# Performance work log

Measured on AMD Instinct MI355X. Metric: run time of the kernel, lower is better.

## Reference

```python
import jax, jax.numpy as jnp
import numpy as np

DEPTH = 2
DIM = 256
MLP = 1024
B = 2
N = 2048


def setup_inputs() -> dict:
    key = jax.random.key(0)
    ks = jax.random.split(key, 6)
    s = 0.02
    d = DIM
    f32 = jnp.float32
    return {
        "x": jax.random.normal(ks[0], (B, N, d), f32),
        "ln1_g": jnp.ones((DEPTH, d), f32),
        "ln1_b": jnp.zeros((DEPTH, d), f32),
        "Wqkv": (jax.random.normal(ks[1], (DEPTH, d, 3 * d), f32) * s),
        "bqkv": jnp.zeros((DEPTH, 3 * d), f32),
        "Wo": (jax.random.normal(ks[2], (DEPTH, d, d), f32) * s),
        "bo": jnp.zeros((DEPTH, d), f32),
        "ln2_g": jnp.ones((DEPTH, d), f32),
        "ln2_b": jnp.zeros((DEPTH, d), f32),
        "W1": (jax.random.normal(ks[3], (DEPTH, d, MLP), f32) * s),
        "b1": jnp.zeros((DEPTH, MLP), f32),
        "W2": (jax.random.normal(ks[4], (DEPTH, MLP, d), f32) * s),
        "b2": jnp.zeros((DEPTH, d), f32),
        "heads": 8,
    }


def _ln(x, g, b, eps=1e-5):
    m = x.mean(-1, keepdims=True)
    v = ((x - m) ** 2).mean(-1, keepdims=True)
    return (x - m) * jax.lax.rsqrt(v + eps) * g + b


def reference(x, ln1_g, ln1_b, Wqkv, bqkv, Wo, bo, ln2_g, ln2_b, W1, b1, W2, b2, heads):
    b, n, dim = x.shape
    hd = dim // heads
    scale = hd ** -0.5
    depth = Wqkv.shape[0]
    out = x
    # NOTE: faithful to original: `x` is never updated inside the loop,
    # so only the last layer's output is returned.
    for i in range(depth):
        y = _ln(x, ln1_g[i], ln1_b[i])
        qkv = y @ Wqkv[i] + bqkv[i]                      # [b,n,3*dim]
        qkv = qkv.reshape(b, n, 3, heads, hd)
        q, k, v = jnp.moveaxis(qkv, 2, 0)                # each [b,n,h,hd]
        q = q.transpose(0, 2, 1, 3)                      # [b,h,n,hd]
        k = k.transpose(0, 2, 1, 3)
        v = v.transpose(0, 2, 1, 3)
        dots = jnp.einsum('bhid,bhjd->bhij', q, k) * scale
        attn = jax.nn.softmax(dots, axis=-1)
        o = jnp.einsum('bhij,bhjd->bhid', attn, v)       # [b,h,n,hd]
        o = o.transpose(0, 2, 1, 3).reshape(b, n, dim)
        o = o @ Wo[i] + bo[i]
        a = o + x                                        # attn residual
        z = _ln(a, ln2_g[i], ln2_b[i])
        m = jax.nn.gelu(z @ W1[i] + b1[i], approximate=False) @ W2[i] + b2[i]
        out = m + a                                      # mlp residual
    return out
```

## Files before the change

### kernel.cpp

```cpp
#include <hip/hip_runtime.h>
#include <hip/hip_bf16.h>
#include <math.h>

#define DEPTHC 2
#define DIMD   256
#define MLPD   1024
#define BB     2
#define NN     2048
#define HH     8
#define HD     32
#define ROWS   (BB * NN)
#define KSPLIT 4

typedef __attribute__((ext_vector_type(8))) short bf16x8;
typedef __attribute__((ext_vector_type(4))) float f32x4;

__device__ __forceinline__ short f2bf(float x) {
    union { float f; unsigned u; } c; c.f = x;
    unsigned u = c.u + (0x7fffu + ((c.u >> 16) & 1u));
    return (short)(u >> 16);
}
__device__ __forceinline__ float bf2f(short s) {
    union { unsigned u; float f; } c; c.u = ((unsigned)(unsigned short)s) << 16;
    return c.f;
}

__global__ __launch_bounds__(256) void prep(
    const float* __restrict__ Wqkv, const float* __restrict__ Wo,
    const float* __restrict__ W1,   const float* __restrict__ W2,
    short* __restrict__ WqkvF, short* __restrict__ WoF,
    short* __restrict__ W1F,   short* __restrict__ W2F,
    const float* __restrict__ x, const float* __restrict__ g,
    const float* __restrict__ be, short* __restrict__ y)
{
    __shared__ short Ts[128][72];

    if (blockIdx.x >= 96) {
        const int wave = threadIdx.x >> 6;
        const int lane = threadIdx.x & 63;
        const int row  = (blockIdx.x - 96) * 4 + wave;
        const int c    = lane * 4;

        const float4 v = *(const float4*)&x[(size_t)row * DIMD + c];
        float s  = v.x + v.y + v.z + v.w;
        float sq = v.x * v.x + v.y * v.y + v.z * v.z + v.w * v.w;
#pragma unroll
        for (int off = 32; off > 0; off >>= 1) {
            s  += __shfl_down(s,  off, 64);
            sq += __shfl_down(sq, off, 64);
        }
        s  = __shfl(s,  0, 64);
        sq = __shfl(sq, 0, 64);

        const float mean = s * (1.f / DIMD);
        const float var  = sq * (1.f / DIMD) - mean * mean;
        const float rstd = rsqrtf(var + 1e-5f);

        const float4 gg = *(const float4*)&g[c];
        const float4 bb = *(const float4*)&be[c];
        short4 ov;
        ov.x = f2bf((v.x - mean) * rstd * gg.x + bb.x);
        ov.y = f2bf((v.y - mean) * rstd * gg.y + bb.y);
        ov.z = f2bf((v.z - mean) * rstd * gg.z + bb.z);
        ov.w = f2bf((v.w - mean) * rstd * gg.w + bb.w);
        *(short4*)&y[(size_t)row * DIMD + c] = ov;
        return;
    }

    int blk = blockIdx.x;
    const float* W; short* WF; int K, N;
    if (blk < 24)      {           W = Wqkv; WF = WqkvF; K = 256;  N = 768;  }
    else if (blk < 32) { blk -= 24; W = Wo;   WF = WoF;   K = 256;  N = 256;  }
    else if (blk < 64) { blk -= 32; W = W1;   WF = W1F;   K = 256;  N = 1024; }
    else               { blk -= 64; W = W2;   WF = W2F;   K = 1024; N = 256;  }
    const int nkc = K >> 7;
    const int bx  = blk / nkc;
    const int kc  = blk % nkc;
    const int n0  = bx * 64;
    const int k0  = kc * 128;

    const int nc  = threadIdx.x & 63;
    const int kr0 = threadIdx.x >> 6;
#pragma unroll
    for (int i = 0; i < 32; ++i) {
        const int kr = kr0 + i * 4;
        Ts[kr][nc] = f2bf(W[(size_t)(k0 + kr) * N + n0 + nc]);
    }
    __syncthreads();

    short* out = WF + ((size_t)bx * nkc + kc) * 8192;
#pragma unroll
    for (int i = 0; i < 4; ++i) {
        const int u    = threadIdx.x + i * 256;
        const int l16  = u & 15;
        const int quad = (u >> 4) & 3;
        const int nt   = (u >> 6) & 3;
        const int ks   = (u >> 8) & 3;
        const int n    = nt * 16 + l16;
        const int kk   = (ks * 4 + quad) * 8;
        bf16x8 v;
#pragma unroll
        for (int j = 0; j < 8; ++j) v[j] = Ts[kk + j][n];
        *(bf16x8*)&out[(size_t)u * 8] = v;
    }
}

template <int K, bool GELU, bool RES, bool OBF, bool VTG, bool MERGE>
__global__ __launch_bounds__(256) void gemm_ks(
    const short* __restrict__ A, const short* __restrict__ WF,
    const float* __restrict__ bias, const float* __restrict__ R,
    void* __restrict__ Cv, int N, short* __restrict__ vtg,
    const short* __restrict__ pO, const float* __restrict__ pl)
{
    __shared__ short smem[4][4096];

    const int tid  = threadIdx.x;
    const int w    = tid >> 6;
    const int lane = tid & 63;
    const int quad = lane >> 4;
    const int l16  = lane & 15;
    const int n0   = blockIdx.x * 64;
    const int m0   = blockIdx.y * 64;
    constexpr int NKC   = K / 128;
    constexpr int SLICE = K / 4;
    constexpr int NHC   = SLICE / 64;

    const short* wfb  = WF + (size_t)blockIdx.x * NKC * 8192;
    const short* arow = (MERGE ? pO : A) ? ((MERGE ? pO : A) + (size_t)(m0 + l16) * K + quad * 8)
                                         : nullptr;
    short* reg = smem[w];

    f32x4 acc[4][4] = {};

#pragma unroll
    for (int hc = 0; hc < NHC; ++hc) {
        const int kbase = w * SLICE + hc * 64;
        const short* src = wfb +
            ((size_t)(kbase >> 7) * 1024 + (size_t)((kbase >> 6) & 1) * 512) * 8;
#pragma unroll
        for (int i = 0; i < 8; ++i)
            *(bf16x8*)&reg[(i * 64 + lane) * 8] =
                *(const bf16x8*)&src[(size_t)(i * 64 + lane) * 8];

#pragma unroll
        for (int ksl = 0; ksl < 2; ++ksl) {
            const int kk = kbase + ksl * 32;
            bf16x8 af[4];
#pragma unroll
            for (int mt = 0; mt < 4; ++mt) {
                if (!MERGE) {
                    af[mt] = *(const bf16x8*)(arow + (size_t)mt * 16 * K + kk);
                } else {
                    const int row = m0 + l16 + mt * 16;
                    const int c   = kk + quad * 8;
                    const int h   = c >> 5;
                    const int d0  = c & 31;
                    const int b   = row >> 11;
                    const int q   = row & (NN - 1);
                    const size_t rg = ((size_t)(b * HH + h) * NN + q) * KSPLIT;
                    const float L = pl[rg] + pl[rg + 1] + pl[rg + 2] + pl[rg + 3];
                    float o[8] = {};
#pragma unroll
                    for (int s = 0; s < KSPLIT; ++s) {
                        const bf16x8 t = *(const bf16x8*)&pO[(rg + s) * HD + d0];
#pragma unroll
                        for (int j = 0; j < 8; ++j) o[j] += bf2f(t[j]);
                    }
                    const float inv = 1.f / L;
#pragma unroll
                    for (int j = 0; j < 8; ++j) af[mt][j] = f2bf(o[j] * inv);
                }
            }
#pragma unroll
            for (int nt = 0; nt < 4; ++nt) {
                const bf16x8 bf = *(const bf16x8*)
                    &reg[(((ksl * 4 + nt) * 4 + quad) * 16 + l16) * 8];
#pragma unroll
                for (int mt = 0; mt < 4; ++mt)
                    acc[mt][nt] = __builtin_amdgcn_mfma_f32_16x16x32_bf16(
                        af[mt], bf, acc[mt][nt], 0, 0, 0);
            }
        }
    }

#pragma unroll
    for (int p = 0; p < 2; ++p) {
        __syncthreads();
#pragma unroll
        for (int mtl = 0; mtl < 2; ++mtl)
#pragma unroll
            for (int nt = 0; nt < 4; ++nt)
                *(f32x4*)&smem[w][((mtl * 4 + nt) * 64 + lane) * 8] = acc[2 * p + mtl][nt];
        __syncthreads();
        if ((w >> 1) == p) {
            const int mtl = w & 1;
            const int mt  = 2 * p + mtl;
#pragma unroll
            for (int nt = 0; nt < 4; ++nt) {
                const int idx = ((mtl * 4 + nt) * 64 + lane) * 8;
                const f32x4 s0 = *(const f32x4*)&smem[0][idx];
                const f32x4 s1 = *(const f32x4*)&smem[1][idx];
                const f32x4 s2 = *(const f32x4*)&smem[2][idx];
                const f32x4 s3 = *(const f32x4*)&smem[3][idx];
                const f32x4 s  = (s0 + s1) + (s2 + s3);
                const int col  = n0 + nt * 16 + l16;
                const float bb = bias[col];
#pragma unroll
                for (int r = 0; r < 4; ++r) {
                    const int row = m0 + mt * 16 + quad * 4 + r;
                    float v = s[r] + bb;
                    if (RES)  v += R[(size_t)row * N + col];
                    if (GELU) v = 0.5f * v * (1.f + erff(v * 0.70710678118f));
                    const short bv = f2bf(v);
                    if (OBF) ((short*)Cv)[(size_t)row * N + col] = bv;
                    else     ((float*)Cv)[(size_t)row * N + col] = v;
                    if (VTG && n0 >= 2 * DIMD) {
                        const int vc = col - 2 * DIMD;
                        const int b  = row >> 11;
                        const int q  = row & (NN - 1);
                        const int h  = vc >> 5;
                        const int d  = vc & 31;
                        vtg[((size_t)(b * HH + h) * HD + d) * NN + q] = bv;
                    }
                }
            }
        }
    }
}

__global__ __launch_bounds__(256) void ln_kernel(
    const float* __restrict__ x, const float* __restrict__ g,
    const float* __restrict__ bta, short* __restrict__ y)
{
    const int wave = threadIdx.x >> 6;
    const int lane = threadIdx.x & 63;
    const int row  = blockIdx.x * 4 + wave;
    const int c    = lane * 4;

    const float4 v = *(const float4*)&x[(size_t)row * DIMD + c];
    float s  = v.x + v.y + v.z + v.w;
    float sq = v.x * v.x + v.y * v.y + v.z * v.z + v.w * v.w;
#pragma unroll
    for (int off = 32; off > 0; off >>= 1) {
        s  += __shfl_down(s,  off, 64);
        sq += __shfl_down(sq, off, 64);
    }
    s  = __shfl(s,  0, 64);
    sq = __shfl(sq, 0, 64);

    const float mean = s * (1.f / DIMD);
    const float var  = sq * (1.f / DIMD) - mean * mean;
    const float rstd = rsqrtf(var + 1e-5f);

    const float4 gg = *(const float4*)&g[c];
    const float4 bb = *(const float4*)&bta[c];
    short4 ov;
    ov.x = f2bf((v.x - mean) * rstd * gg.x + bb.x);
    ov.y = f2bf((v.y - mean) * rstd * gg.y + bb.y);
    ov.z = f2bf((v.z - mean) * rstd * gg.z + bb.z);
    ov.w = f2bf((v.w - mean) * rstd * gg.w + bb.w);
    *(short4*)&y[(size_t)row * DIMD + c] = ov;
}

__global__ __launch_bounds__(256) void attn_mfma(
    const short* __restrict__ qkv, const short* __restrict__ vtg,
    short* __restrict__ pO, float* __restrict__ pl)
{
    __shared__ short Ks[64][40];
    __shared__ short Vs[32][72];
    __shared__ short Ps[4][16][72];

    const int tid  = threadIdx.x;
    const int w    = tid >> 6;
    const int lane = tid & 63;
    const int quad = lane >> 4;
    const int l16  = lane & 15;
    const int bh   = blockIdx.y;
    const int b    = bh >> 3;
    const int h    = bh & 7;
    const int ks   = blockIdx.z;
    const int q0   = blockIdx.x * 64 + w * 16;

    const float scale2 = 0.25504606868000365f;
    const short* base = qkv + (size_t)b * NN * (3 * DIMD);

    const bf16x8 qfrag =
        *(const bf16x8*)(base + (size_t)(q0 + l16) * (3 * DIMD) + h * HD + quad * 8);

    const int skey = tid >> 2;
    const int sd   = (tid & 3) * 8;
    const int vd   = tid >> 3;
    const int vk   = (tid & 7) * 8;

    const short* kgp = base + (size_t)(ks * (NN / KSPLIT) + skey) * (3 * DIMD)
                       + DIMD + h * HD + sd;
    const short* vgp = vtg + ((size_t)bh * HD + vd) * NN
                       + ks * (NN / KSPLIT) + vk;

    f32x4 oacc0 = {0.f, 0.f, 0.f, 0.f};
    f32x4 oacc1 = {0.f, 0.f, 0.f, 0.f};
    float rowsum[4] = {0.f, 0.f, 0.f, 0.f};

    bf16x8 kreg = *(const bf16x8*)kgp;
    bf16x8 vreg = *(const bf16x8*)vgp;

#pragma unroll 1
    for (int t = 0; t < NN / KSPLIT / 64; ++t) {
        __syncthreads();
        *(bf16x8*)&Ks[skey][sd] = kreg;
        *(bf16x8*)&Vs[vd][vk]   = vreg;
        __syncthreads();

        if (t + 1 < NN / KSPLIT / 64) {
            kreg = *(const bf16x8*)(kgp + (size_t)(t + 1) * 64 * (3 * DIMD));
            vreg = *(const bf16x8*)(vgp + (t + 1) * 64);
        }

        f32x4 s[4];
#pragma unroll
        for (int kt = 0; kt < 4; ++kt) {
            const bf16x8 kf = *(const bf16x8*)&Ks[kt * 16 + l16][quad * 8];
            f32x4 z = {0.f, 0.f, 0.f, 0.f};
            s[kt] = __builtin_amdgcn_mfma_f32_16x16x32_bf16(qfrag, kf, z, 0, 0, 0);
        }

#pragma unroll
        for (int kt = 0; kt < 4; ++kt)
#pragma unroll
            for (int r = 0; r < 4; ++r) {
                const float p = exp2f(fmaf(s[kt][r], scale2, -16.f));
                rowsum[r] += p;
                union { float f; unsigned u; } cv; cv.f = p;
                Ps[w][quad * 4 + r][kt * 16 + l16] = (short)(cv.u >> 16);
            }

#pragma unroll
        for (int c = 0; c < 2; ++c) {
            const bf16x8 pf = *(const bf16x8*)&Ps[w][l16][c * 32 + quad * 8];
            const bf16x8 v0 = *(const bf16x8*)&Vs[l16][c * 32 + quad * 8];
            const bf16x8 v1 = *(const bf16x8*)&Vs[16 + l16][c * 32 + quad * 8];
            oacc0 = __builtin_amdgcn_mfma_f32_16x16x32_bf16(pf, v0, oacc0, 0, 0, 0);
            oacc1 = __builtin_amdgcn_mfma_f32_16x16x32_bf16(pf, v1, oacc1, 0, 0, 0);
        }
    }

#pragma unroll
    for (int off = 1; off <= 8; off <<= 1)
#pragma unroll
        for (int r = 0; r < 4; ++r)
            rowsum[r] += __shfl_xor(rowsum[r], off, 64);

#pragma unroll
    for (int r = 0; r < 4; ++r) {
        const size_t rg = (size_t)bh * NN + q0 + quad * 4 + r;
        pO[(rg * KSPLIT + ks) * HD + l16]      = f2bf(oacc0[r]);
        pO[(rg * KSPLIT + ks) * HD + 16 + l16] = f2bf(oacc1[r]);
        if (l16 == 0) pl[rg * KSPLIT + ks] = rowsum[r];
    }
}

extern "C" void kernel_launch(void* const* d_in, const int* in_sizes, int n_in,
                              void* d_out, int out_size, void* d_ws, size_t ws_size,
                              hipStream_t stream)
{
    const int L = DEPTHC - 1;
    const float* x     = (const float*)d_in[0];
    const float* ln1_g = (const float*)d_in[1]  + L * DIMD;
    const float* ln1_b = (const float*)d_in[2]  + L * DIMD;
    const float* Wqkv  = (const float*)d_in[3]  + (size_t)L * DIMD * 3 * DIMD;
    const float* bqkv  = (const float*)d_in[4]  + L * 3 * DIMD;
    const float* Wo    = (const float*)d_in[5]  + (size_t)L * DIMD * DIMD;
    const float* bo    = (const float*)d_in[6]  + L * DIMD;
    const float* ln2_g = (const float*)d_in[7]  + L * DIMD;
    const float* ln2_b = (const float*)d_in[8]  + L * DIMD;
    const float* W1    = (const float*)d_in[9]  + (size_t)L * DIMD * MLPD;
    const float* b1    = (const float*)d_in[10] + L * MLPD;
    const float* W2    = (const float*)d_in[11] + (size_t)L * MLPD * DIMD;
    const float* b2    = (const float*)d_in[12] + L * DIMD;
    float* out = (float*)d_out;

    short* WqkvF = (short*)d_ws;
    short* WoF   = WqkvF + 12 * 2 * 8192;
    short* W1F   = WoF   + 4 * 2 * 8192;
    short* W2F   = W1F   + 16 * 2 * 8192;
    short* ybf   = W2F   + 4 * 8 * 8192;
    short* zbf   = ybf   + (size_t)ROWS * DIMD;
    short* qkvbf = zbf   + (size_t)ROWS * DIMD;
    short* vtg   = qkvbf + (size_t)ROWS * 3 * DIMD;
    short* pO    = vtg   + (size_t)16 * HD * NN;
    short* m1bf  = pO    + (size_t)16 * NN * KSPLIT * HD;
    float* pl    = (float*)(m1bf + (size_t)ROWS * MLPD);
    float* a     = pl + (size_t)16 * NN * KSPLIT;

    prep<<<96 + ROWS / 4, 256, 0, stream>>>(
        Wqkv, Wo, W1, W2, WqkvF, WoF, W1F, W2F, x, ln1_g, ln1_b, ybf);

    gemm_ks<256, false, false, true, true, false><<<dim3(12, 64), 256, 0, stream>>>(
        ybf, WqkvF, bqkv, nullptr, qkvbf, 3 * DIMD, vtg, nullptr, nullptr);

    attn_mfma<<<dim3(NN / 64, BB * HH, KSPLIT), 256, 0, stream>>>(qkvbf, vtg, pO, pl);

    gemm_ks<256, false, true, false, false, true><<<dim3(4, 64), 256, 0, stream>>>(
        nullptr, WoF, bo, x, a, DIMD, nullptr, pO, pl);

    ln_kernel<<<ROWS / 4, 256, 0, stream>>>(a, ln2_g, ln2_b, zbf);

    gemm_ks<256, true, false, true, false, false><<<dim3(16, 64), 256, 0, stream>>>(
        zbf, W1F, b1, nullptr, m1bf, MLPD, nullptr, nullptr, nullptr);

    gemm_ks<1024, false, true, false, false, false><<<dim3(4, 64), 256, 0, stream>>>(
        m1bf, W2F, b2, a, out, DIMD, nullptr, nullptr, nullptr);
}
```

Before: 169.1 us.

## Fuse attention merge, out-proj, LN2 and MLP into one tail kernel

Replaces the four post-attention launches (Wo GEMM with split-K merge, LN2, W1 GEMM with GELU, W2 GEMM) with a single kernel that handles 32 rows per block. The residual, the LN2 output and the GELU activations stay in registers and LDS. This removes the global round trips for a, zbf and the 4096x1024 m1 intermediate, along with three launches. In exchange there are only 128 blocks, so per-CU parallelism is lower, and every block re-streams all of Wo, W1 and W2 from global memory.

```diff
diff --git a/kernel.cpp b/kernel.cpp
--- a/kernel.cpp
+++ b/kernel.cpp
@@ -11,6 +11,7 @@
 #define HD     32
 #define ROWS   (BB * NN)
 #define KSPLIT 4
+#define TM     32
 
 typedef __attribute__((ext_vector_type(8))) short bf16x8;
 typedef __attribute__((ext_vector_type(4))) float f32x4;
@@ -105,14 +106,13 @@
     }
 }
 
-template <int K, bool GELU, bool RES, bool OBF, bool VTG, bool MERGE>
-__global__ __launch_bounds__(256) void gemm_ks(
+__global__ __launch_bounds__(256) void gemm_qkv(
     const short* __restrict__ A, const short* __restrict__ WF,
-    const float* __restrict__ bias, const float* __restrict__ R,
-    void* __restrict__ Cv, int N, short* __restrict__ vtg,
-    const short* __restrict__ pO, const float* __restrict__ pl)
+    const float* __restrict__ bias, short* __restrict__ Cv,
+    short* __restrict__ vtg)
 {
     __shared__ short smem[4][4096];
+    constexpr int K = 256, N = 3 * DIMD;
 
     const int tid  = threadIdx.x;
     const int w    = tid >> 6;
@@ -121,56 +121,28 @@
     const int l16  = lane & 15;
     const int n0   = blockIdx.x * 64;
     const int m0   = blockIdx.y * 64;
-    constexpr int NKC   = K / 128;
-    constexpr int SLICE = K / 4;
-    constexpr int NHC   = SLICE / 64;
-
-    const short* wfb  = WF + (size_t)blockIdx.x * NKC * 8192;
-    const short* arow = (MERGE ? pO : A) ? ((MERGE ? pO : A) + (size_t)(m0 + l16) * K + quad * 8)
-                                         : nullptr;
+
+    const short* wfb  = WF + (size_t)blockIdx.x * 2 * 8192;
+    const short* arow = A + (size_t)(m0 + l16) * K + quad * 8;
     short* reg = smem[w];
 
     f32x4 acc[4][4] = {};
 
-#pragma unroll
-    for (int hc = 0; hc < NHC; ++hc) {
-        const int kbase = w * SLICE + hc * 64;
-        const short* src = wfb +
-            ((size_t)(kbase >> 7) * 1024 + (size_t)((kbase >> 6) & 1) * 512) * 8;
+    {
+        const int kbase = w * 64;
+        const short* src = wfb + ((size_t)(kbase >> 7) * 1024
+                                  + (size_t)((kbase >> 6) & 1) * 512) * 8;
 #pragma unroll
         for (int i = 0; i < 8; ++i)
             *(bf16x8*)&reg[(i * 64 + lane) * 8] =
                 *(const bf16x8*)&src[(size_t)(i * 64 + lane) * 8];
-
 #pragma unroll
         for (int ksl = 0; ksl < 2; ++ksl) {
             const int kk = kbase + ksl * 32;
             bf16x8 af[4];
 #pragma unroll
-            for (int mt = 0; mt < 4; ++mt) {
-                if (!MERGE) {
-                    af[mt] = *(const bf16x8*)(arow + (size_t)mt * 16 * K + kk);
-                } else {
-                    const int row = m0 + l16 + mt * 16;
-                    const int c   = kk + quad * 8;
-                    const int h   = c >> 5;
-                    const int d0  = c & 31;
-                    const int b   = row >> 11;
-                    const int q   = row & (NN - 1);
-                    const size_t rg = ((size_t)(b * HH + h) * NN + q) * KSPLIT;
-                    const float L = pl[rg] + pl[rg + 1] + pl[rg + 2] + pl[rg + 3];
-                    float o[8] = {};
-#pragma unroll
-                    for (int s = 0; s < KSPLIT; ++s) {
-                        const bf16x8 t = *(const bf16x8*)&pO[(rg + s) * HD + d0];
-#pragma unroll
-                        for (int j = 0; j < 8; ++j) o[j] += bf2f(t[j]);
-                    }
-                    const float inv = 1.f / L;
-#pragma unroll
-                    for (int j = 0; j < 8; ++j) af[mt][j] = f2bf(o[j] * inv);
-                }
-            }
+            for (int mt = 0; mt < 4; ++mt)
+                af[mt] = *(const bf16x8*)(arow + (size_t)mt * 16 * K + kk);
 #pragma unroll
             for (int nt = 0; nt < 4; ++nt) {
                 const bf16x8 bf = *(const bf16x8*)
@@ -208,58 +180,18 @@
 #pragma unroll
                 for (int r = 0; r < 4; ++r) {
                     const int row = m0 + mt * 16 + quad * 4 + r;
-                    float v = s[r] + bb;
-                    if (RES)  v += R[(size_t)row * N + col];
-                    if (GELU) v = 0.5f * v * (1.f + erff(v * 0.70710678118f));
-                    const short bv = f2bf(v);
-                    if (OBF) ((short*)Cv)[(size_t)row * N + col] = bv;
-                    else     ((float*)Cv)[(size_t)row * N + col] = v;
-                    if (VTG && n0 >= 2 * DIMD) {
+                    const short bv = f2bf(s[r] + bb);
+                    Cv[(size_t)row * N + col] = bv;
+                    if (n0 >= 2 * DIMD) {
                         const int vc = col - 2 * DIMD;
                         const int b  = row >> 11;
                         const int q  = row & (NN - 1);
-                        const int h  = vc >> 5;
-                        const int d  = vc & 31;
-                        vtg[((size_t)(b * HH + h) * HD + d) * NN + q] = bv;
+                        vtg[((size_t)(b * HH + (vc >> 5)) * HD + (vc & 31)) * NN + q] = bv;
                     }
                 }
             }
         }
     }
-}
-
-__global__ __launch_bounds__(256) void ln_kernel(
-    const float* __restrict__ x, const float* __restrict__ g,
-    const float* __restrict__ bta, short* __restrict__ y)
-{
-    const int wave = threadIdx.x >> 6;
-    const int lane = threadIdx.x & 63;
-    const int row  = blockIdx.x * 4 + wave;
-    const int c    = lane * 4;
-
-    const float4 v = *(const float4*)&x[(size_t)row * DIMD + c];
-    float s  = v.x + v.y + v.z + v.w;
-    float sq = v.x * v.x + v.y * v.y + v.z * v.z + v.w * v.w;
-#pragma unroll
-    for (int off = 32; off > 0; off >>= 1) {
-        s  += __shfl_down(s,  off, 64);
-        sq += __shfl_down(sq, off, 64);
-    }
-    s  = __shfl(s,  0, 64);
-    sq = __shfl(sq, 0, 64);
-
-    const float mean = s * (1.f / DIMD);
-    const float var  = sq * (1.f / DIMD) - mean * mean;
-    const float rstd = rsqrtf(var + 1e-5f);
-
-    const float4 gg = *(const float4*)&g[c];
-    const float4 bb = *(const float4*)&bta[c];
-    short4 ov;
-    ov.x = f2bf((v.x - mean) * rstd * gg.x + bb.x);
-    ov.y = f2bf((v.y - mean) * rstd * gg.y + bb.y);
-    ov.z = f2bf((v.z - mean) * rstd * gg.z + bb.z);
-    ov.w = f2bf((v.w - mean) * rstd * gg.w + bb.w);
-    *(short4*)&y[(size_t)row * DIMD + c] = ov;
 }
 
 __global__ __launch_bounds__(256) void attn_mfma(
@@ -356,6 +288,208 @@
         pO[(rg * KSPLIT + ks) * HD + l16]      = f2bf(oacc0[r]);
         pO[(rg * KSPLIT + ks) * HD + 16 + l16] = f2bf(oacc1[r]);
         if (l16 == 0) pl[rg * KSPLIT + ks] = rowsum[r];
+    }
+}
+
+__global__ __launch_bounds__(256) void tail(
+    const short* __restrict__ pO, const float* __restrict__ pl,
+    const float* __restrict__ x,
+    const short* __restrict__ WoF, const float* __restrict__ bo,
+    const float* __restrict__ ln2g, const float* __restrict__ ln2b,
+    const short* __restrict__ W1F, const float* __restrict__ b1,
+    const short* __restrict__ W2F, const float* __restrict__ b2,
+    float* __restrict__ out)
+{
+    __shared__ short zs[TM][264];
+    __shared__ short ms[4][TM][68];
+    __shared__ short bs[4][2048];
+    __shared__ float stats[2][4][TM];
+
+    const int tid  = threadIdx.x;
+    const int w    = tid >> 6;
+    const int lane = tid & 63;
+    const int quad = lane >> 4;
+    const int l16  = lane & 15;
+    const int m0   = blockIdx.x * TM;
+
+#pragma unroll
+    for (int i = 0; i < 4; ++i) {
+        const int u   = tid + i * 256;
+        const int row = u >> 5;
+        const int cc  = u & 31;
+        const int h   = cc >> 2;
+        const int d0  = (cc & 3) * 8;
+        const int grow = m0 + row;
+        const int b = grow >> 11, q = grow & (NN - 1);
+        const size_t rg = ((size_t)(b * HH + h) * NN + q) * KSPLIT;
+        const float L = pl[rg] + pl[rg + 1] + pl[rg + 2] + pl[rg + 3];
+        float o[8] = {};
+#pragma unroll
+        for (int s = 0; s < KSPLIT; ++s) {
+            const bf16x8 t = *(const bf16x8*)&pO[(rg + s) * HD + d0];
+#pragma unroll
+            for (int j = 0; j < 8; ++j) o[j] += bf2f(t[j]);
+        }
+        const float inv = 1.f / L;
+        bf16x8 z8;
+#pragma unroll
+        for (int j = 0; j < 8; ++j) z8[j] = f2bf(o[j] * inv);
+        *(bf16x8*)&zs[row][cc * 8] = z8;
+    }
+    __syncthreads();
+
+    f32x4 acc1[2][4] = {};
+#pragma unroll
+    for (int kk = 0; kk < 256; kk += 32) {
+        const short* src = WoF + ((size_t)w * 2 + (kk >> 7)) * 8192
+                           + (size_t)((kk >> 5) & 3) * 2048;
+#pragma unroll
+        for (int i = 0; i < 4; ++i)
+            *(bf16x8*)&bs[w][(i * 64 + lane) * 8] =
+                *(const bf16x8*)&src[(size_t)(i * 64 + lane) * 8];
+        bf16x8 af[2];
+#pragma unroll
+        for (int mt = 0; mt < 2; ++mt)
+            af[mt] = *(const bf16x8*)&zs[l16 + mt * 16][kk + quad * 8];
+#pragma unroll
+        for (int nt = 0; nt < 4; ++nt) {
+            const bf16x8 bf = *(const bf16x8*)&bs[w][((nt * 4 + quad) * 16 + l16) * 8];
+#pragma unroll
+            for (int mt = 0; mt < 2; ++mt)
+                acc1[mt][nt] = __builtin_amdgcn_mfma_f32_16x16x32_bf16(
+                    af[mt], bf, acc1[mt][nt], 0, 0, 0);
+        }
+    }
+
+    float a_reg[2][4][4];
+    float bov[4], gv[4], bev[4];
+#pragma unroll
+    for (int nt = 0; nt < 4; ++nt) {
+        const int col = w * 64 + nt * 16 + l16;
+        bov[nt] = bo[col];
+        gv[nt]  = ln2g[col];
+        bev[nt] = ln2b[col];
+    }
+#pragma unroll
+    for (int mt = 0; mt < 2; ++mt)
+#pragma unroll
+    for (int r = 0; r < 4; ++r) {
+        const int grow = m0 + mt * 16 + quad * 4 + r;
+        float s = 0.f, sq = 0.f;
+#pragma unroll
+        for (int nt = 0; nt < 4; ++nt) {
+            const float v = acc1[mt][nt][r] + bov[nt]
+                          + x[(size_t)grow * DIMD + w * 64 + nt * 16 + l16];
+            a_reg[mt][r][nt] = v;
+            s += v; sq += v * v;
+        }
+#pragma unroll
+        for (int off = 1; off <= 8; off <<= 1) {
+            s  += __shfl_xor(s,  off, 64);
+            sq += __shfl_xor(sq, off, 64);
+        }
+        if (l16 == 0) {
+            stats[0][w][mt * 16 + quad * 4 + r] = s;
+            stats[1][w][mt * 16 + quad * 4 + r] = sq;
+        }
+    }
+    __syncthreads();
+
+#pragma unroll
+    for (int mt = 0; mt < 2; ++mt)
+#pragma unroll
+    for (int r = 0; r < 4; ++r) {
+        const int lrow = mt * 16 + quad * 4 + r;
+        const float s  = stats[0][0][lrow] + stats[0][1][lrow]
+                       + stats[0][2][lrow] + stats[0][3][lrow];
+        const float sq = stats[1][0][lrow] + stats[1][1][lrow]
+                       + stats[1][2][lrow] + stats[1][3][lrow];
+        const float mean = s * (1.f / DIMD);
+        const float var  = sq * (1.f / DIMD) - mean * mean;
+        const float rstd = rsqrtf(var + 1e-5f);
+#pragma unroll
+        for (int nt = 0; nt < 4; ++nt)
+            zs[lrow][w * 64 + nt * 16 + l16] =
+                f2bf((a_reg[mt][r][nt] - mean) * rstd * gv[nt] + bev[nt]);
+    }
+    __syncthreads();
+
+    f32x4 acc2[2][4] = {};
+#pragma unroll 1
+    for (int rd = 0; rd < 4; ++rd) {
+        const int st = rd * 4 + w;
+        f32x4 accm[2][4] = {};
+#pragma unroll
+        for (int kk = 0; kk < 256; kk += 32) {
+            const short* src = W1F + ((size_t)st * 2 + (kk >> 7)) * 8192
+                               + (size_t)((kk >> 5) & 3) * 2048;
+#pragma unroll
+            for (int i = 0; i < 4; ++i)
+                *(bf16x8*)&bs[w][(i * 64 + lane) * 8] =
+                    *(const bf16x8*)&src[(size_t)(i * 64 + lane) * 8];
+            bf16x8 af[2];
+#pragma unroll
+            for (int mt = 0; mt < 2; ++mt)
+                af[mt] = *(const bf16x8*)&zs[l16 + mt * 16][kk + quad * 8];
+#pragma unroll
+            for (int nt = 0; nt < 4; ++nt) {
+                const bf16x8 bf = *(const bf16x8*)&bs[w][((nt * 4 + quad) * 16 + l16) * 8];
+#pragma unroll
+                for (int mt = 0; mt < 2; ++mt)
+                    accm[mt][nt] = __builtin_amdgcn_mfma_f32_16x16x32_bf16(
+                        af[mt], bf, accm[mt][nt], 0, 0, 0);
+            }
+        }
+#pragma unroll
+        for (int mt = 0; mt < 2; ++mt)
+#pragma unroll
+        for (int nt = 0; nt < 4; ++nt)
+#pragma unroll
+        for (int r = 0; r < 4; ++r) {
+            float v = accm[mt][nt][r] + b1[st * 64 + nt * 16 + l16];
+            v = 0.5f * v * (1.f + erff(v * 0.70710678118f));
+            ms[w][mt * 16 + quad * 4 + r][nt * 16 + l16] = f2bf(v);
+        }
+        __syncthreads();
+
+#pragma unroll
+        for (int j = 0; j < 4; ++j)
+#pragma unroll
+        for (int ksl = 0; ksl < 2; ++ksl) {
+            const int kglob = (rd * 4 + j) * 64 + ksl * 32;
+            const short* src = W2F + ((size_t)w * 8 + (kglob >> 7)) * 8192
+                               + (size_t)((kglob >> 5) & 3) * 2048;
+#pragma unroll
+            for (int i = 0; i < 4; ++i)
+                *(bf16x8*)&bs[w][(i * 64 + lane) * 8] =
+                    *(const bf16x8*)&src[(size_t)(i * 64 + lane) * 8];
+            bf16x8 af[2];
+#pragma unroll
+            for (int mt = 0; mt < 2; ++mt)
+                af[mt] = *(const bf16x8*)&ms[j][l16 + mt * 16][ksl * 32 + quad * 8];
+#pragma unroll
+            for (int nt = 0; nt < 4; ++nt) {
+                const bf16x8 bf = *(const bf16x8*)&bs[w][((nt * 4 + quad) * 16 + l16) * 8];
+#pragma unroll
+                for (int mt = 0; mt < 2; ++mt)
+                    acc2[mt][nt] = __builtin_amdgcn_mfma_f32_16x16x32_bf16(
+                        af[mt], bf, acc2[mt][nt], 0, 0, 0);
+            }
+        }
+        __syncthreads();
+    }
+
+#pragma unroll
+    for (int mt = 0; mt < 2; ++mt)
+#pragma unroll
+    for (int nt = 0; nt < 4; ++nt) {
+        const int col = w * 64 + nt * 16 + l16;
+        const float bb = b2[col];
+#pragma unroll
+        for (int r = 0; r < 4; ++r) {
+            const int grow = m0 + mt * 16 + quad * 4 + r;
+            out[(size_t)grow * DIMD + col] = acc2[mt][nt][r] + bb + a_reg[mt][r][nt];
+        }
     }
 }
 
@@ -384,30 +518,18 @@
     short* W1F   = WoF   + 4 * 2 * 8192;
     short* W2F   = W1F   + 16 * 2 * 8192;
     short* ybf   = W2F   + 4 * 8 * 8192;
-    short* zbf   = ybf   + (size_t)ROWS * DIMD;
-    short* qkvbf = zbf   + (size_t)ROWS * DIMD;
+    short* qkvbf = ybf   + (size_t)ROWS * DIMD;
     short* vtg   = qkvbf + (size_t)ROWS * 3 * DIMD;
     short* pO    = vtg   + (size_t)16 * HD * NN;
-    short* m1bf  = pO    + (size_t)16 * NN * KSPLIT * HD;
-    float* pl    = (float*)(m1bf + (size_t)ROWS * MLPD);
-    float* a     = pl + (size_t)16 * NN * KSPLIT;
+    float* pl    = (float*)(pO + (size_t)16 * NN * KSPLIT * HD);
 
     prep<<<96 + ROWS / 4, 256, 0, stream>>>(
         Wqkv, Wo, W1, W2, WqkvF, WoF, W1F, W2F, x, ln1_g, ln1_b, ybf);
 
-    gemm_ks<256, false, false, true, true, false><<<dim3(12, 64), 256, 0, stream>>>(
-        ybf, WqkvF, bqkv, nullptr, qkvbf, 3 * DIMD, vtg, nullptr, nullptr);
+    gemm_qkv<<<dim3(12, 64), 256, 0, stream>>>(ybf, WqkvF, bqkv, qkvbf, vtg);
 
     attn_mfma<<<dim3(NN / 64, BB * HH, KSPLIT), 256, 0, stream>>>(qkvbf, vtg, pO, pl);
 
-    gemm_ks<256, false, true, false, false, true><<<dim3(4, 64), 256, 0, stream>>>(
-        nullptr, WoF, bo, x, a, DIMD, nullptr, pO, pl);
-
-    ln_kernel<<<ROWS / 4, 256, 0, stream>>>(a, ln2_g, ln2_b, zbf);
-
-    gemm_ks<256, true, false, true, false, false><<<dim3(16, 64), 256, 0, stream>>>(
-        zbf, W1F, b1, nullptr, m1bf, MLPD, nullptr, nullptr, nullptr);
-
-    gemm_ks<1024, false, true, false, false, false><<<dim3(4, 64), 256, 0, stream>>>(
-        m1bf, W2F, b2, a, out, DIMD, nullptr, nullptr, nullptr);
-}
+    tail<<<ROWS / TM, 256, 0, stream>>>(
+        pO, pl, x, WoF, bo, ln2_g, ln2_b, W1F, b1, W2F, b2, out);
+}
```

After: 216.0 us. 27.7% more time.
